# Kernel tuning notes

Measured on AMD Instinct MI355X. Metric: run time of the kernel, lower is better.

The kernel has to match this reference:

```python
import jax, jax.numpy as jnp
import numpy as np

TEMP = 0.2
EPS = 1e-12


def _l2norm(v, axis=1):
    n = jnp.linalg.norm(v, axis=axis, keepdims=True)
    return v / jnp.maximum(n, EPS)


def setup_inputs() -> dict:
    key = jax.random.key(0)
    ks = jax.random.split(key, 7)
    B, D, P, K = 2048, 256, 100, 30
    return {
        "x": jax.random.normal(ks[0], (B, D), jnp.float32),
        "x_aug": jax.random.normal(ks[1], (B, D), jnp.float32),
        "proto_w": jax.random.normal(ks[2], (P, D), jnp.float32),
        "hard_q1": jax.random.randint(ks[3], (B,), 0, P, jnp.int32),
        "hard_q2": jax.random.randint(ks[4], (B,), 0, P, jnp.int32),
        "neg_q1": jax.random.randint(ks[5], (B, K), 0, P, jnp.int32),
        "neg_q2": jax.random.randint(ks[6], (B, K), 0, P, jnp.int32),
    }


def reference(x, x_aug, proto_w, hard_q1, hard_q2, neg_q1, neg_q2):
    B = x.shape[0]
    N = 2 * B
    P = proto_w.shape[0]

    out1 = _l2norm(x)                          # [B, D]
    out2 = _l2norm(x_aug)                      # [B, D]
    out = jnp.concatenate([out1, out2], axis=0)  # [N, D]
    hard_q = jnp.concatenate([hard_q1, hard_q2], axis=0)  # [N]
    neg_q = jnp.concatenate([neg_q1, neg_q2], axis=0)     # [N, K]

    sim = jnp.exp(jnp.matmul(out, out.T) / TEMP)  # [N, N]
    eye = jnp.eye(N, dtype=bool)

    # hard_selection: mask[i,j] = (i != j) and (hard_q[j] in neg_q[i])
    # build per-row prototype membership table [N, P] to avoid a [N, K, N] blowup
    member = jnp.zeros((N, P), dtype=bool).at[jnp.arange(N)[:, None], neg_q].set(True)
    mask = (~eye) & member[:, hard_q]  # member[i, hard_q[j]] -> [N, N]

    # sample_reweighting
    w = _l2norm(proto_w)                # normalized prototypes [P, D]
    proto_dist = jnp.matmul(w, w.T)     # cosine similarity [P, P]
    R = proto_dist[hard_q[:, None], hard_q[None, :]]  # [N, N]
    R = jnp.where(eye, 0.0, R)          # diag is 0 when the row min is taken
    rmin = jnp.min(R, axis=1, keepdims=True)
    R = jnp.where(eye, rmin, R)         # reweight[i][i] = min(reweight[i])
    rmax = jnp.max(R, axis=1, keepdims=True)
    R = (R - rmin) / (rmax - rmin)      # per-row min-max normalize
    mu = jnp.mean(R, axis=1, keepdims=True)
    std = jnp.std(R, axis=1, ddof=1, keepdims=True)  # torch.std is unbiased
    reweight = jnp.exp((R - mu) ** 2 / (2.0 * std ** 2))
    sim = sim * reweight

    # masked_select(...).sum() == global sum over masked entries (scalar)
    total = jnp.sum(jnp.where(mask, sim, 0.0))

    pos = jnp.exp(jnp.sum(out1 * out2, axis=-1) / TEMP)  # [B]
    pos = jnp.concatenate([pos, pos], axis=0)            # [N]
    loss = jnp.mean(-jnp.log(pos / total))
    return loss
```

## Files before the change

kernel.cpp:

```cpp
#include <hip/hip_runtime.h>
#include <hip/hip_bf16.h>
#include <cstdint>

#define B_ 2048
#define N_ 4096
#define D_ 256
#define P_ 100
#define K_ 30
#define INVT 5.0f

typedef __attribute__((ext_vector_type(8))) short bf16x8;
typedef __attribute__((ext_vector_type(4))) float f32x4;

__device__ __forceinline__ float waveReduceSum(float v) {
#pragma unroll
  for (int off = 32; off > 0; off >>= 1) v += __shfl_xor(v, off, 64);
  return v;
}

__device__ __forceinline__ float blockReduceSum256(float v, float* s4) {
  int lane = threadIdx.x & 63, w = threadIdx.x >> 6;
  v = waveReduceSum(v);
  __syncthreads();
  if (lane == 0) s4[w] = v;
  __syncthreads();
  return s4[0] + s4[1] + s4[2] + s4[3];
}

__global__ void init_kernel(float* sums) {
  if (threadIdx.x < 2) sums[threadIdx.x] = 0.f;
}

__global__ void norm_kernel(const float* __restrict__ x, const float* __restrict__ xa,
                            __hip_bfloat16* __restrict__ outb, float* __restrict__ sums) {
  __shared__ float s4[4];
  int i = blockIdx.x, t = threadIdx.x;
  float a = x[i * D_ + t];
  float ss = blockReduceSum256(a * a, s4);
  float o1 = a / fmaxf(sqrtf(ss), 1e-12f);
  outb[i * D_ + t] = __float2bfloat16(o1);
  float b = xa[i * D_ + t];
  float ss2 = blockReduceSum256(b * b, s4);
  float o2 = b / fmaxf(sqrtf(ss2), 1e-12f);
  outb[(B_ + i) * D_ + t] = __float2bfloat16(o2);
  float d = blockReduceSum256(o1 * o2, s4);
  if (t == 0) atomicAdd(&sums[1], d);
}

__global__ void pnorm_kernel(const float* __restrict__ pw, float* __restrict__ w) {
  __shared__ float s4[4];
  int p = blockIdx.x, t = threadIdx.x;
  float a = pw[p * D_ + t];
  float ss = blockReduceSum256(a * a, s4);
  w[p * D_ + t] = a / fmaxf(sqrtf(ss), 1e-12f);
}

__global__ void pd_kernel(const float* __restrict__ w, float* __restrict__ pd) {
  __shared__ float wq[D_];
  int q = blockIdx.x, t = threadIdx.x, lane = t & 63, wv = t >> 6;
  wq[t] = w[q * D_ + t];
  __syncthreads();
  for (int r = wv; r < P_; r += 4) {
    const float* wr = w + r * D_;
    float s = 0.f;
#pragma unroll
    for (int e = 0; e < 4; ++e) s += wq[lane * 4 + e] * wr[lane * 4 + e];
    s = waveReduceSum(s);
    if (lane == 0) pd[q * P_ + r] = s;
  }
}

__global__ void hist_kernel(const int* __restrict__ hq1, const int* __restrict__ hq2,
                            int* __restrict__ hq, int* __restrict__ cnt) {
  __shared__ int c[P_];
  int t = threadIdx.x;
  if (t < P_) c[t] = 0;
  __syncthreads();
  for (int i = t; i < N_; i += 256) {
    int q = (i < B_) ? hq1[i] : hq2[i - B_];
    hq[i] = q;
    atomicAdd(&c[q], 1);
  }
  __syncthreads();
  if (t < P_) cnt[t] = c[t];
}

__global__ void gtab_kernel(const int* __restrict__ hq, const int* __restrict__ cnt,
                            const float* __restrict__ pd, const int* __restrict__ nq1,
                            const int* __restrict__ nq2, float* __restrict__ gtab) {
  __shared__ unsigned char memb[4][104];
  int wv = threadIdx.x >> 6, lane = threadIdx.x & 63;
  int i = blockIdx.x * 4 + wv;
  int q = hq[i];
  if (lane < 52) { memb[wv][lane * 2] = 0; memb[wv][lane * 2 + 1] = 0; }
  __syncthreads();
  const int* nrow = (i < B_) ? (nq1 + i * K_) : (nq2 + (i - B_) * K_);
  if (lane < K_) memb[wv][nrow[lane]] = 1;
  __syncthreads();

  int p0 = lane, p1 = lane + 64;
  bool has1 = (p1 < P_);
  float v0 = pd[q * P_ + p0];
  int m0 = cnt[p0] - (p0 == q ? 1 : 0);
  float v1 = 0.f; int m1 = 0;
  if (has1) { v1 = pd[q * P_ + p1]; m1 = cnt[p1] - (p1 == q ? 1 : 0); }

  float mn = 1e30f, mx = -1e30f;
  if (m0 > 0) { mn = fminf(mn, v0); mx = fmaxf(mx, v0); }
  if (has1 && m1 > 0) { mn = fminf(mn, v1); mx = fmaxf(mx, v1); }
#pragma unroll
  for (int off = 32; off > 0; off >>= 1) {
    mn = fminf(mn, __shfl_xor(mn, off, 64));
    mx = fmaxf(mx, __shfl_xor(mx, off, 64));
  }
  float rmin = fminf(0.f, mn);
  float rmax = fmaxf(rmin, mx);
  float inv = 1.f / (rmax - rmin);
  float r0 = (v0 - rmin) * inv, r1 = (v1 - rmin) * inv;
  float s1 = (m0 > 0 ? (float)m0 * r0 : 0.f) + ((has1 && m1 > 0) ? (float)m1 * r1 : 0.f);
  s1 = waveReduceSum(s1);
  float mu = s1 / (float)N_;
  float ss = (m0 > 0 ? (float)m0 * (r0 - mu) * (r0 - mu) : 0.f) +
             ((has1 && m1 > 0) ? (float)m1 * (r1 - mu) * (r1 - mu) : 0.f);
  ss = waveReduceSum(ss);
  ss += mu * mu;
  float var = ss / (float)(N_ - 1);
  float i2v = 1.f / (2.f * var);
  float g0 = memb[wv][p0] ? __expf((r0 - mu) * (r0 - mu) * i2v) : 0.f;
  gtab[i * P_ + p0] = g0;
  if (has1) {
    float g1 = memb[wv][p1] ? __expf((r1 - mu) * (r1 - mu) * i2v) : 0.f;
    gtab[i * P_ + p1] = g1;
  }
}

__device__ __forceinline__ void gload16(void* ldsdst, const void* gsrc) {
  __builtin_amdgcn_global_load_lds(
      (const __attribute__((address_space(1))) unsigned int*)gsrc,
      (__attribute__((address_space(3))) unsigned int*)ldsdst, 16, 0, 0);
}

__global__ __launch_bounds__(512, 2) void tot_kernel(
    const __hip_bfloat16* __restrict__ outb, const float* __restrict__ gtab,
    const int* __restrict__ hq, float* __restrict__ sums) {
  __shared__ __align__(16) char lds[65536];
  const int tid = threadIdx.x, lane = tid & 63, wid = tid >> 6;
  const int i0 = blockIdx.y * 128, j0 = blockIdx.x * 128;
  const int wr = wid >> 2, wc = wid & 3;

  f32x4 acc[4][2] = {};

  const int wseg = wid & 3;
  const bool isB = (wid >= 4);
  const int growbase = isB ? j0 : i0;
  char* panel = lds + (isB ? 32768 : 0);

  for (int kk = 0; kk < 2; ++kk) {
#pragma unroll
    for (int it = 0; it < 8; ++it) {
      int rbase = wseg * 32 + it * 4;
      int row = rbase + (lane >> 4);
      int c = lane & 15;
      int src = (growbase + row) * D_ + kk * 128 + ((c ^ (row & 7)) * 8);
      gload16(panel + rbase * 256, outb + src);
    }
    __syncthreads();
#pragma unroll
    for (int ks = 0; ks < 4; ++ks) {
      bf16x8 af[4], bf[2];
#pragma unroll
      for (int m = 0; m < 4; ++m) {
        int row = wr * 64 + m * 16 + (lane & 15);
        int off = row * 256 + ((((ks << 2) + (lane >> 4)) ^ (row & 7)) << 4);
        af[m] = *(const bf16x8*)(lds + off);
      }
#pragma unroll
      for (int n = 0; n < 2; ++n) {
        int row = wc * 32 + n * 16 + (lane & 15);
        int off = 32768 + row * 256 + ((((ks << 2) + (lane >> 4)) ^ (row & 7)) << 4);
        bf[n] = *(const bf16x8*)(lds + off);
      }
#pragma unroll
      for (int m = 0; m < 4; ++m)
#pragma unroll
        for (int n = 0; n < 2; ++n)
          acc[m][n] = __builtin_amdgcn_mfma_f32_16x16x32_bf16(af[m], bf[n], acc[m][n], 0, 0, 0);
    }
    __syncthreads();
  }

  int jc = j0 + wc * 32 + (lane & 15);
  int hqa = hq[jc], hqb = hq[jc + 16];
  float local = 0.f;
#pragma unroll
  for (int m = 0; m < 4; ++m) {
    int ib = i0 + wr * 64 + m * 16 + ((lane >> 4) << 2);
#pragma unroll
    for (int r = 0; r < 4; ++r) {
      int i = ib + r;
      const float* grow = gtab + i * P_;
      float sa = acc[m][0][r];
      if (i != jc) local += grow[hqa] * __expf(sa * INVT);
      float sb = acc[m][1][r];
      if (i != jc + 16) local += grow[hqb] * __expf(sb * INVT);
    }
  }
  local = waveReduceSum(local);
  __shared__ float s8[8];
  if (lane == 0) s8[wid] = local;
  __syncthreads();
  if (tid == 0) {
    float t = 0.f;
#pragma unroll
    for (int w = 0; w < 8; ++w) t += s8[w];
    atomicAdd(&sums[0], t);
  }
}

__global__ void finish_kernel(const float* __restrict__ sums, float* __restrict__ out) {
  out[0] = logf(sums[0]) - sums[1] * (INVT / (float)B_);
}

extern "C" void kernel_launch(void* const* d_in, const int* in_sizes, int n_in,
                              void* d_out, int out_size, void* d_ws, size_t ws_size,
                              hipStream_t stream) {
  const float* x   = (const float*)d_in[0];
  const float* xa  = (const float*)d_in[1];
  const float* pw  = (const float*)d_in[2];
  const int* hq1   = (const int*)d_in[3];
  const int* hq2   = (const int*)d_in[4];
  const int* nq1   = (const int*)d_in[5];
  const int* nq2   = (const int*)d_in[6];
  float* out = (float*)d_out;

  char* ws = (char*)d_ws;
  __hip_bfloat16* outb = (__hip_bfloat16*)(ws);
  float* gtab = (float*)(ws + 2097152);
  float* w    = (float*)(ws + 2097152 + 1638400);
  float* pd   = (float*)(ws + 2097152 + 1638400 + 102400);
  int*   hq   = (int*)  (ws + 2097152 + 1638400 + 102400 + 40064);
  int*   cnt  = (int*)  (ws + 2097152 + 1638400 + 102400 + 40064 + 16384);
  float* sums = (float*)(ws + 2097152 + 1638400 + 102400 + 40064 + 16384 + 512);

  init_kernel<<<1, 64, 0, stream>>>(sums);
  norm_kernel<<<B_, 256, 0, stream>>>(x, xa, outb, sums);
  pnorm_kernel<<<P_, 256, 0, stream>>>(pw, w);
  pd_kernel<<<P_, 256, 0, stream>>>(w, pd);
  hist_kernel<<<1, 256, 0, stream>>>(hq1, hq2, hq, cnt);
  gtab_kernel<<<N_ / 4, 256, 0, stream>>>(hq, cnt, pd, nq1, nq2, gtab);
  tot_kernel<<<dim3(32, 32), 512, 0, stream>>>(outb, gtab, hq, sums);
  finish_kernel<<<1, 1, 0, stream>>>(sums, out);
}
```

Before: 154.9 us.

## Exploit Gram symmetry with upper-triangular tiles, stage bf16 weight table in LDS, fuse prep kernels

The main tot kernel now launches only the 528 upper-triangular 128x128 tiles of the symmetric Gram matrix. Each off-diagonal tile adds both the (i,j) and (j,i) weights, which roughly halves the MFMA and exp work. The per-row reweight table is stored as bf16 and copied into LDS per tile, replacing scattered global gathers. The small setup kernels (init, histogram, prototype norm, prototype dot products, row normalisation) are merged into two launches, and normalisation is vectorised with one wave per row. The costs are bf16 rounding of the weights, a serial loop to decode the triangular tile index, and an extra LDS staging pass.

```diff
diff --git a/kernel.cpp b/kernel.cpp
--- a/kernel.cpp
+++ b/kernel.cpp
@@ -11,6 +11,7 @@
 
 typedef __attribute__((ext_vector_type(8))) short bf16x8;
 typedef __attribute__((ext_vector_type(4))) float f32x4;
+typedef __attribute__((ext_vector_type(4))) unsigned short us4;
 
 __device__ __forceinline__ float waveReduceSum(float v) {
 #pragma unroll
@@ -27,67 +28,83 @@
   return s4[0] + s4[1] + s4[2] + s4[3];
 }
 
-__global__ void init_kernel(float* sums) {
-  if (threadIdx.x < 2) sums[threadIdx.x] = 0.f;
-}
-
-__global__ void norm_kernel(const float* __restrict__ x, const float* __restrict__ xa,
-                            __hip_bfloat16* __restrict__ outb, float* __restrict__ sums) {
+__device__ __forceinline__ unsigned short f2bf(float f) {
+  __hip_bfloat16 h = __float2bfloat16(f);
+  return *reinterpret_cast<unsigned short*>(&h);
+}
+__device__ __forceinline__ float bf2f(unsigned short u) {
+  return __uint_as_float(((unsigned int)u) << 16);
+}
+
+__global__ void prep_kernel(const float* __restrict__ pw, const int* __restrict__ hq1,
+                            const int* __restrict__ hq2, int* __restrict__ hq,
+                            int* __restrict__ cnt, float* __restrict__ pninv,
+                            float* __restrict__ sums) {
+  __shared__ int c[P_];
   __shared__ float s4[4];
-  int i = blockIdx.x, t = threadIdx.x;
-  float a = x[i * D_ + t];
-  float ss = blockReduceSum256(a * a, s4);
-  float o1 = a / fmaxf(sqrtf(ss), 1e-12f);
-  outb[i * D_ + t] = __float2bfloat16(o1);
-  float b = xa[i * D_ + t];
-  float ss2 = blockReduceSum256(b * b, s4);
-  float o2 = b / fmaxf(sqrtf(ss2), 1e-12f);
-  outb[(B_ + i) * D_ + t] = __float2bfloat16(o2);
-  float d = blockReduceSum256(o1 * o2, s4);
-  if (t == 0) atomicAdd(&sums[1], d);
-}
-
-__global__ void pnorm_kernel(const float* __restrict__ pw, float* __restrict__ w) {
+  int t = threadIdx.x;
+  if (blockIdx.x == 0) {
+    if (t < 2) sums[t] = 0.f;
+    if (t < P_) c[t] = 0;
+    __syncthreads();
+    for (int i = t; i < N_; i += 256) {
+      int q = (i < B_) ? hq1[i] : hq2[i - B_];
+      hq[i] = q;
+      atomicAdd(&c[q], 1);
+    }
+    __syncthreads();
+    if (t < P_) cnt[t] = c[t];
+  } else {
+    int r = blockIdx.x - 1;
+    float a = pw[r * D_ + t];
+    float ss = blockReduceSum256(a * a, s4);
+    if (t == 0) pninv[r] = 1.f / fmaxf(sqrtf(ss), 1e-12f);
+  }
+}
+
+__global__ void normpd_kernel(const float* __restrict__ x, const float* __restrict__ xa,
+                              const float* __restrict__ pw, const float* __restrict__ pninv,
+                              __hip_bfloat16* __restrict__ outb, float* __restrict__ pd,
+                              float* __restrict__ sums) {
   __shared__ float s4[4];
-  int p = blockIdx.x, t = threadIdx.x;
-  float a = pw[p * D_ + t];
-  float ss = blockReduceSum256(a * a, s4);
-  w[p * D_ + t] = a / fmaxf(sqrtf(ss), 1e-12f);
-}
-
-__global__ void pd_kernel(const float* __restrict__ w, float* __restrict__ pd) {
   __shared__ float wq[D_];
-  int q = blockIdx.x, t = threadIdx.x, lane = t & 63, wv = t >> 6;
-  wq[t] = w[q * D_ + t];
-  __syncthreads();
-  for (int r = wv; r < P_; r += 4) {
-    const float* wr = w + r * D_;
-    float s = 0.f;
-#pragma unroll
-    for (int e = 0; e < 4; ++e) s += wq[lane * 4 + e] * wr[lane * 4 + e];
-    s = waveReduceSum(s);
-    if (lane == 0) pd[q * P_ + r] = s;
-  }
-}
-
-__global__ void hist_kernel(const int* __restrict__ hq1, const int* __restrict__ hq2,
-                            int* __restrict__ hq, int* __restrict__ cnt) {
-  __shared__ int c[P_];
-  int t = threadIdx.x;
-  if (t < P_) c[t] = 0;
-  __syncthreads();
-  for (int i = t; i < N_; i += 256) {
-    int q = (i < B_) ? hq1[i] : hq2[i - B_];
-    hq[i] = q;
-    atomicAdd(&c[q], 1);
-  }
-  __syncthreads();
-  if (t < P_) cnt[t] = c[t];
+  int t = threadIdx.x, lane = t & 63, wv = t >> 6;
+  if (blockIdx.x < 512) {
+    int i = blockIdx.x * 4 + wv;
+    float4 a = ((const float4*)(x + i * D_))[lane];
+    float ss = waveReduceSum(a.x * a.x + a.y * a.y + a.z * a.z + a.w * a.w);
+    float inv1 = 1.f / fmaxf(sqrtf(ss), 1e-12f);
+    float o1x = a.x * inv1, o1y = a.y * inv1, o1z = a.z * inv1, o1w = a.w * inv1;
+    us4 p1; p1[0] = f2bf(o1x); p1[1] = f2bf(o1y); p1[2] = f2bf(o1z); p1[3] = f2bf(o1w);
+    ((us4*)(outb + i * D_))[lane] = p1;
+    float4 b = ((const float4*)(xa + i * D_))[lane];
+    float ss2 = waveReduceSum(b.x * b.x + b.y * b.y + b.z * b.z + b.w * b.w);
+    float inv2 = 1.f / fmaxf(sqrtf(ss2), 1e-12f);
+    float o2x = b.x * inv2, o2y = b.y * inv2, o2z = b.z * inv2, o2w = b.w * inv2;
+    us4 p2; p2[0] = f2bf(o2x); p2[1] = f2bf(o2y); p2[2] = f2bf(o2z); p2[3] = f2bf(o2w);
+    ((us4*)(outb + (B_ + i) * D_))[lane] = p2;
+    float d = waveReduceSum(o1x * o2x + o1y * o2y + o1z * o2z + o1w * o2w);
+    if (lane == 0) s4[wv] = d;
+    __syncthreads();
+    if (t == 0) atomicAdd(&sums[1], s4[0] + s4[1] + s4[2] + s4[3]);
+  } else {
+    int q = blockIdx.x - 512;
+    wq[t] = pw[q * D_ + t];
+    __syncthreads();
+    float nq = pninv[q];
+    for (int r = wv; r < P_; r += 4) {
+      float4 b = ((const float4*)(pw + r * D_))[lane];
+      float s = wq[lane * 4] * b.x + wq[lane * 4 + 1] * b.y +
+                wq[lane * 4 + 2] * b.z + wq[lane * 4 + 3] * b.w;
+      s = waveReduceSum(s);
+      if (lane == 0) pd[q * P_ + r] = s * nq * pninv[r];
+    }
+  }
 }
 
 __global__ void gtab_kernel(const int* __restrict__ hq, const int* __restrict__ cnt,
                             const float* __restrict__ pd, const int* __restrict__ nq1,
-                            const int* __restrict__ nq2, float* __restrict__ gtab) {
+                            const int* __restrict__ nq2, unsigned short* __restrict__ gtabh) {
   __shared__ unsigned char memb[4][104];
   int wv = threadIdx.x >> 6, lane = threadIdx.x & 63;
   int i = blockIdx.x * 4 + wv;
@@ -127,10 +144,10 @@
   float var = ss / (float)(N_ - 1);
   float i2v = 1.f / (2.f * var);
   float g0 = memb[wv][p0] ? __expf((r0 - mu) * (r0 - mu) * i2v) : 0.f;
-  gtab[i * P_ + p0] = g0;
+  gtabh[i * P_ + p0] = f2bf(g0);
   if (has1) {
     float g1 = memb[wv][p1] ? __expf((r1 - mu) * (r1 - mu) * i2v) : 0.f;
-    gtab[i * P_ + p1] = g1;
+    gtabh[i * P_ + p1] = f2bf(g1);
   }
 }
 
@@ -141,11 +158,17 @@
 }
 
 __global__ __launch_bounds__(512, 2) void tot_kernel(
-    const __hip_bfloat16* __restrict__ outb, const float* __restrict__ gtab,
+    const __hip_bfloat16* __restrict__ outb, const unsigned short* __restrict__ gtabh,
     const int* __restrict__ hq, float* __restrict__ sums) {
   __shared__ __align__(16) char lds[65536];
+  __shared__ float s8[8];
   const int tid = threadIdx.x, lane = tid & 63, wid = tid >> 6;
-  const int i0 = blockIdx.y * 128, j0 = blockIdx.x * 128;
+
+  int rem = blockIdx.x, bi = 0;
+  while (rem >= 32 - bi) { rem -= 32 - bi; ++bi; }
+  const int bj = bi + rem;
+  const bool offdiag = (bi != bj);
+  const int i0 = bi * 128, j0 = bj * 128;
   const int wr = wid >> 2, wc = wid & 3;
 
   f32x4 acc[4][2] = {};
@@ -167,7 +190,7 @@
     __syncthreads();
 #pragma unroll
     for (int ks = 0; ks < 4; ++ks) {
-      bf16x8 af[4], bf[2];
+      bf16x8 af[4], bfr[2];
 #pragma unroll
       for (int m = 0; m < 4; ++m) {
         int row = wr * 64 + m * 16 + (lane & 15);
@@ -178,35 +201,56 @@
       for (int n = 0; n < 2; ++n) {
         int row = wc * 32 + n * 16 + (lane & 15);
         int off = 32768 + row * 256 + ((((ks << 2) + (lane >> 4)) ^ (row & 7)) << 4);
-        bf[n] = *(const bf16x8*)(lds + off);
+        bfr[n] = *(const bf16x8*)(lds + off);
       }
 #pragma unroll
       for (int m = 0; m < 4; ++m)
 #pragma unroll
         for (int n = 0; n < 2; ++n)
-          acc[m][n] = __builtin_amdgcn_mfma_f32_16x16x32_bf16(af[m], bf[n], acc[m][n], 0, 0, 0);
-    }
-    __syncthreads();
-  }
-
-  int jc = j0 + wc * 32 + (lane & 15);
-  int hqa = hq[jc], hqb = hq[jc + 16];
+          acc[m][n] = __builtin_amdgcn_mfma_f32_16x16x32_bf16(af[m], bfr[n], acc[m][n], 0, 0, 0);
+    }
+    __syncthreads();
+  }
+
+  unsigned short* ga = (unsigned short*)lds;
+  unsigned short* gb = (unsigned short*)(lds + 26624);
+  int* hqA = (int*)(lds + 53248);
+  int* hqB = (int*)(lds + 53760);
+  for (int idx = tid; idx < 128 * P_; idx += 512) {
+    int r = idx / P_, c = idx - r * P_;
+    ga[r * 104 + c] = gtabh[(i0 + r) * P_ + c];
+    gb[r * 104 + c] = gtabh[(j0 + r) * P_ + c];
+  }
+  if (tid < 128) hqA[tid] = hq[i0 + tid];
+  else if (tid < 256) hqB[tid - 128] = hq[j0 + tid - 128];
+  __syncthreads();
+
+  const int jl0 = wc * 32 + (lane & 15);
+  const int jl1 = jl0 + 16;
+  const int hj0 = hqB[jl0], hj1 = hqB[jl1];
   float local = 0.f;
 #pragma unroll
   for (int m = 0; m < 4; ++m) {
-    int ib = i0 + wr * 64 + m * 16 + ((lane >> 4) << 2);
+    int ilb = wr * 64 + m * 16 + ((lane >> 4) << 2);
 #pragma unroll
     for (int r = 0; r < 4; ++r) {
-      int i = ib + r;
-      const float* grow = gtab + i * P_;
-      float sa = acc[m][0][r];
-      if (i != jc) local += grow[hqa] * __expf(sa * INVT);
-      float sb = acc[m][1][r];
-      if (i != jc + 16) local += grow[hqb] * __expf(sb * INVT);
+      int il = ilb + r;
+      float e0 = __expf(acc[m][0][r] * INVT);
+      float e1 = __expf(acc[m][1][r] * INVT);
+      float wa0 = bf2f(ga[il * 104 + hj0]);
+      float wa1 = bf2f(ga[il * 104 + hj1]);
+      if (offdiag) {
+        int hi = hqA[il];
+        float wb0 = bf2f(gb[jl0 * 104 + hi]);
+        float wb1 = bf2f(gb[jl1 * 104 + hi]);
+        local += (wa0 + wb0) * e0 + (wa1 + wb1) * e1;
+      } else {
+        if (il != jl0) local += wa0 * e0;
+        if (il != jl1) local += wa1 * e1;
+      }
     }
   }
   local = waveReduceSum(local);
-  __shared__ float s8[8];
   if (lane == 0) s8[wid] = local;
   __syncthreads();
   if (tid == 0) {
@@ -234,20 +278,17 @@
   float* out = (float*)d_out;
 
   char* ws = (char*)d_ws;
-  __hip_bfloat16* outb = (__hip_bfloat16*)(ws);
-  float* gtab = (float*)(ws + 2097152);
-  float* w    = (float*)(ws + 2097152 + 1638400);
-  float* pd   = (float*)(ws + 2097152 + 1638400 + 102400);
-  int*   hq   = (int*)  (ws + 2097152 + 1638400 + 102400 + 40064);
-  int*   cnt  = (int*)  (ws + 2097152 + 1638400 + 102400 + 40064 + 16384);
-  float* sums = (float*)(ws + 2097152 + 1638400 + 102400 + 40064 + 16384 + 512);
-
-  init_kernel<<<1, 64, 0, stream>>>(sums);
-  norm_kernel<<<B_, 256, 0, stream>>>(x, xa, outb, sums);
-  pnorm_kernel<<<P_, 256, 0, stream>>>(pw, w);
-  pd_kernel<<<P_, 256, 0, stream>>>(w, pd);
-  hist_kernel<<<1, 256, 0, stream>>>(hq1, hq2, hq, cnt);
-  gtab_kernel<<<N_ / 4, 256, 0, stream>>>(hq, cnt, pd, nq1, nq2, gtab);
-  tot_kernel<<<dim3(32, 32), 512, 0, stream>>>(outb, gtab, hq, sums);
+  __hip_bfloat16* outb  = (__hip_bfloat16*)(ws);
+  unsigned short* gtabh = (unsigned short*)(ws + 2097152);
+  float* pd    = (float*)(ws + 2916352);
+  float* pninv = (float*)(ws + 2956352);
+  int*   hq    = (int*)  (ws + 2956800);
+  int*   cnt   = (int*)  (ws + 2973184);
+  float* sums  = (float*)(ws + 2973696);
+
+  prep_kernel<<<101, 256, 0, stream>>>(pw, hq1, hq2, hq, cnt, pninv, sums);
+  normpd_kernel<<<612, 256, 0, stream>>>(x, xa, pw, pninv, outb, pd, sums);
+  gtab_kernel<<<N_ / 4, 256, 0, stream>>>(hq, cnt, pd, nq1, nq2, gtabh);
+  tot_kernel<<<528, 512, 0, stream>>>(outb, gtabh, hq, sums);
   finish_kernel<<<1, 1, 0, stream>>>(sums, out);
 }
```

Measured after the change: 126.1 us. 18.6% less time.
